# Kernel tuning notes

Measured on AMD Instinct MI355X. Metric: run time of the kernel, lower is better.

Reference implementation:

```python
import jax, jax.numpy as jnp
import numpy as np

C, D, N = 4096, 256, 262144

def setup_inputs() -> dict:
    key = jax.random.key(0)
    k1, k2, k3 = jax.random.split(key, 3)
    centers = jax.random.normal(k1, (C, D), dtype=jnp.float32)
    features = jax.random.normal(k2, (N, D), dtype=jnp.float32)
    labels = jax.random.randint(k3, (N,), 0, C, dtype=jnp.int64)
    return {"centers": centers, "features": features, "labels": labels}

def reference(centers, features, labels):
    # centers: [C, D]; features: [N, D] (unused in forward math); labels: [N]
    c = centers.shape[0]
    sq = jnp.sum(centers * centers, axis=1)                 # [C]
    gram = centers @ centers.T                              # [C, C]
    # pairwise squared euclidean distances; diagonal is exactly 0 analytically
    dist = sq[:, None] + sq[None, :] - 2.0 * gram           # [C, C]
    # centerDist[i] = sum_{j != i} ||c_j - c_i||^2 / (C - 1)
    center_dist = (dist.sum(axis=1) - jnp.diagonal(dist)) / (c - 1)  # [C]
    var = jnp.var(center_dist, ddof=1)                      # torch .var() is unbiased
    return center_dist.sum() / c / var / labels.shape[0]
```

## Files before the change

kernel.cpp:

```cpp
#include <hip/hip_runtime.h>

#define DD 256
#define CC 4096
#define NB 64
#define TPB 1024
#define RPB (CC / NB)
#define D4 (DD / 4)
#define MAGIC 0x05F3A9C1

__global__ __launch_bounds__(TPB) void fused_density(
    const float* __restrict__ centers,
    float* __restrict__ t_part,
    float* __restrict__ S_part,
    double* __restrict__ cd_part,
    double* __restrict__ cd2_part,
    int* __restrict__ flag1,
    int* __restrict__ flag2,
    float* __restrict__ out, long long N) {
  const int tx = threadIdx.x, w = tx >> 6, lane = tx & 63, b = blockIdx.x;

  __shared__ float4 smT[16][64];
  __shared__ float sm2[2][DD];
  __shared__ float smt[DD];
  __shared__ float sSfin;
  __shared__ float sS[16];
  __shared__ double sC[16], sC2[16];
  __shared__ double rc[64], rc2[64];

  const float4* src =
      (const float4*)centers + (size_t)(b * RPB + w * 4) * D4 + lane;
  float4 v0 = src[0 * D4], v1 = src[1 * D4], v2 = src[2 * D4], v3 = src[3 * D4];

  float4 ta;
  ta.x = (v0.x + v1.x) + (v2.x + v3.x);
  ta.y = (v0.y + v1.y) + (v2.y + v3.y);
  ta.z = (v0.z + v1.z) + (v2.z + v3.z);
  ta.w = (v0.w + v1.w) + (v2.w + v3.w);
  smT[w][lane] = ta;
  float ss = (v0.x * v0.x + v0.y * v0.y + v0.z * v0.z + v0.w * v0.w) +
             (v1.x * v1.x + v1.y * v1.y + v1.z * v1.z + v1.w * v1.w) +
             (v2.x * v2.x + v2.y * v2.y + v2.z * v2.z + v2.w * v2.w) +
             (v3.x * v3.x + v3.y * v3.y + v3.z * v3.z + v3.w * v3.w);
  #pragma unroll
  for (int off = 32; off; off >>= 1) ss += __shfl_xor(ss, off, 64);
  if (lane == 0) sS[w] = ss;
  __syncthreads();
  if (tx < 64) {
    float4 s = smT[0][tx];
    #pragma unroll
    for (int k = 1; k < 16; ++k) {
      float4 o = smT[k][tx];
      s.x += o.x; s.y += o.y; s.z += o.z; s.w += o.w;
    }
    ((float4*)t_part)[b * 64 + tx] = s;
  }
  if (tx == 0) {
    float s = 0.f;
    #pragma unroll
    for (int k = 0; k < 16; ++k) s += sS[k];
    S_part[b] = s;
  }
  __syncthreads();
  if (tx == 0)
    __hip_atomic_store(&flag1[b], MAGIC, __ATOMIC_RELEASE,
                       __HIP_MEMORY_SCOPE_AGENT);

  if (tx < NB) {
    while (__hip_atomic_load(&flag1[tx], __ATOMIC_ACQUIRE,
                             __HIP_MEMORY_SCOPE_AGENT) != MAGIC)
      __builtin_amdgcn_s_sleep(1);
  }
  __syncthreads();

  if (tx < 512) {
    const int col = tx & 255, half = tx >> 8;
    const float* tp = t_part + (size_t)half * 32 * DD + col;
    float a0 = 0.f, a1 = 0.f, a2 = 0.f, a3 = 0.f;
    float a4 = 0.f, a5 = 0.f, a6 = 0.f, a7 = 0.f;
    #pragma unroll
    for (int p = 0; p < 32; p += 8) {
      a0 += tp[(p + 0) * DD]; a1 += tp[(p + 1) * DD];
      a2 += tp[(p + 2) * DD]; a3 += tp[(p + 3) * DD];
      a4 += tp[(p + 4) * DD]; a5 += tp[(p + 5) * DD];
      a6 += tp[(p + 6) * DD]; a7 += tp[(p + 7) * DD];
    }
    sm2[half][col] = ((a0 + a1) + (a2 + a3)) + ((a4 + a5) + (a6 + a7));
  } else if (tx >= 512 && tx < 576) {
    float sv = S_part[tx - 512];
    #pragma unroll
    for (int off = 32; off; off >>= 1) sv += __shfl_xor(sv, off, 64);
    if (tx == 512) sSfin = sv;
  }
  __syncthreads();
  if (tx < DD) smt[tx] = sm2[0][tx] + sm2[1][tx];
  __syncthreads();
  const float S = sSfin;
  const float4 t4 = ((const float4*)smt)[lane];

  const float Cf = (float)CC;
  const double inv = 1.0 / (double)(CC - 1);
  double cds = 0.0, cd2 = 0.0;
  #pragma unroll
  for (int r = 0; r < 4; ++r) {
    float4 v = (r == 0) ? v0 : (r == 1) ? v1 : (r == 2) ? v2 : v3;
    float u = (Cf * v.x - 2.f * t4.x) * v.x + (Cf * v.y - 2.f * t4.y) * v.y +
              (Cf * v.z - 2.f * t4.z) * v.z + (Cf * v.w - 2.f * t4.w) * v.w;
    #pragma unroll
    for (int off = 32; off; off >>= 1) u += __shfl_xor(u, off, 64);
    if (lane == 0) {
      double cd = ((double)u + (double)S) * inv;
      cds += cd;
      cd2 += cd * cd;
    }
  }
  if (lane == 0) { sC[w] = cds; sC2[w] = cd2; }
  __syncthreads();
  if (tx == 0) {
    double bc = 0.0, bc2 = 0.0;
    #pragma unroll
    for (int k = 0; k < 16; ++k) { bc += sC[k]; bc2 += sC2[k]; }
    __hip_atomic_store(&cd_part[b], bc, __ATOMIC_RELEASE,
                       __HIP_MEMORY_SCOPE_AGENT);
    __hip_atomic_store(&cd2_part[b], bc2, __ATOMIC_RELEASE,
                       __HIP_MEMORY_SCOPE_AGENT);
    __hip_atomic_store(&flag2[b], MAGIC, __ATOMIC_RELEASE,
                       __HIP_MEMORY_SCOPE_AGENT);
  }

  if (b == 0) {
    if (tx < NB) {
      while (__hip_atomic_load(&flag2[tx], __ATOMIC_ACQUIRE,
                               __HIP_MEMORY_SCOPE_AGENT) != MAGIC)
        __builtin_amdgcn_s_sleep(1);
      rc[tx] = cd_part[tx];
      rc2[tx] = cd2_part[tx];
    }
    __syncthreads();
    #pragma unroll
    for (int st = 32; st; st >>= 1) {
      if (tx < st) { rc[tx] += rc[tx + st]; rc2[tx] += rc2[tx + st]; }
      __syncthreads();
    }
    if (tx == 0) {
      double s = rc[0], s2 = rc2[0];
      double mean = s / (double)CC;
      double var = (s2 - s * s / (double)CC) / (double)(CC - 1);
      out[0] = (float)(mean / var / (double)N);
    }
    if (tx < NB) {
      __hip_atomic_store(&flag1[tx], 0, __ATOMIC_RELEASE,
                         __HIP_MEMORY_SCOPE_AGENT);
      __hip_atomic_store(&flag2[tx], 0, __ATOMIC_RELEASE,
                         __HIP_MEMORY_SCOPE_AGENT);
    }
  }
}

extern "C" void kernel_launch(void* const* d_in, const int* in_sizes, int n_in,
                              void* d_out, int out_size, void* d_ws,
                              size_t ws_size, hipStream_t stream) {
  const float* centers = (const float*)d_in[0];
  long long N = (long long)in_sizes[2];
  (void)n_in; (void)out_size; (void)ws_size;

  char* ws = (char*)d_ws;
  float* t_part = (float*)ws;
  float* S_part = (float*)(ws + 65536);
  double* cd_part = (double*)(ws + 66048);
  double* cd2_part = (double*)(ws + 66560);
  int* flag1 = (int*)(ws + 67072);
  int* flag2 = (int*)(ws + 67328);
  float* outp = (float*)d_out;

  hipLaunchKernelGGL(fused_density, dim3(NB), dim3(TPB), 0, stream, centers,
                     t_part, S_part, cd_part, cd2_part, flag1, flag2, outp, N);
}
```

Before: 16.96 us.

## Use 128 smaller blocks and pack flags with payload in padded cache lines

Doubles the grid to 128 blocks of 512 threads so more CUs load the centers concurrently. Inter-block communication now uses 64-byte-aligned structs that carry each flag next to its payload, which avoids false sharing among flags and lets the payload arrive in the same line as the flag. The cost is a larger grid barrier with twice as many flags to poll, and a longer t_part reduction per thread.

```diff
diff --git a/kernel.cpp b/kernel.cpp
--- a/kernel.cpp
+++ b/kernel.cpp
@@ -2,30 +2,30 @@
 
 #define DD 256
 #define CC 4096
-#define NB 64
-#define TPB 1024
+#define NB 128
+#define TPB 512
 #define RPB (CC / NB)
 #define D4 (DD / 4)
 #define MAGIC 0x05F3A9C1
 
+struct alignas(64) Comm1 { int flag; float S; int pad[14]; };
+struct alignas(64) Comm2 { double cd; double cd2; int flag; int pad[11]; };
+
 __global__ __launch_bounds__(TPB) void fused_density(
     const float* __restrict__ centers,
     float* __restrict__ t_part,
-    float* __restrict__ S_part,
-    double* __restrict__ cd_part,
-    double* __restrict__ cd2_part,
-    int* __restrict__ flag1,
-    int* __restrict__ flag2,
+    Comm1* __restrict__ c1,
+    Comm2* __restrict__ c2,
     float* __restrict__ out, long long N) {
   const int tx = threadIdx.x, w = tx >> 6, lane = tx & 63, b = blockIdx.x;
 
-  __shared__ float4 smT[16][64];
+  __shared__ float4 smT[8][64];
   __shared__ float sm2[2][DD];
   __shared__ float smt[DD];
+  __shared__ float sS[8];
   __shared__ float sSfin;
-  __shared__ float sS[16];
-  __shared__ double sC[16], sC2[16];
-  __shared__ double rc[64], rc2[64];
+  __shared__ double sC[8], sC2[8];
+  __shared__ double rc[NB], rc2[NB];
 
   const float4* src =
       (const float4*)centers + (size_t)(b * RPB + w * 4) * D4 + lane;
@@ -48,7 +48,7 @@
   if (tx < 64) {
     float4 s = smT[0][tx];
     #pragma unroll
-    for (int k = 1; k < 16; ++k) {
+    for (int k = 1; k < 8; ++k) {
       float4 o = smT[k][tx];
       s.x += o.x; s.y += o.y; s.z += o.z; s.w += o.w;
     }
@@ -57,42 +57,44 @@
   if (tx == 0) {
     float s = 0.f;
     #pragma unroll
-    for (int k = 0; k < 16; ++k) s += sS[k];
-    S_part[b] = s;
+    for (int k = 0; k < 8; ++k) s += sS[k];
+    c1[b].S = s;
   }
   __syncthreads();
   if (tx == 0)
-    __hip_atomic_store(&flag1[b], MAGIC, __ATOMIC_RELEASE,
+    __hip_atomic_store(&c1[b].flag, MAGIC, __ATOMIC_RELEASE,
                        __HIP_MEMORY_SCOPE_AGENT);
 
   if (tx < NB) {
-    while (__hip_atomic_load(&flag1[tx], __ATOMIC_ACQUIRE,
+    while (__hip_atomic_load(&c1[tx].flag, __ATOMIC_ACQUIRE,
                              __HIP_MEMORY_SCOPE_AGENT) != MAGIC)
       __builtin_amdgcn_s_sleep(1);
   }
   __syncthreads();
 
-  if (tx < 512) {
+  {
     const int col = tx & 255, half = tx >> 8;
-    const float* tp = t_part + (size_t)half * 32 * DD + col;
+    const float* tp = t_part + (size_t)(half * 64) * DD + col;
     float a0 = 0.f, a1 = 0.f, a2 = 0.f, a3 = 0.f;
     float a4 = 0.f, a5 = 0.f, a6 = 0.f, a7 = 0.f;
     #pragma unroll
-    for (int p = 0; p < 32; p += 8) {
+    for (int p = 0; p < 64; p += 8) {
       a0 += tp[(p + 0) * DD]; a1 += tp[(p + 1) * DD];
       a2 += tp[(p + 2) * DD]; a3 += tp[(p + 3) * DD];
       a4 += tp[(p + 4) * DD]; a5 += tp[(p + 5) * DD];
       a6 += tp[(p + 6) * DD]; a7 += tp[(p + 7) * DD];
     }
     sm2[half][col] = ((a0 + a1) + (a2 + a3)) + ((a4 + a5) + (a6 + a7));
-  } else if (tx >= 512 && tx < 576) {
-    float sv = S_part[tx - 512];
-    #pragma unroll
-    for (int off = 32; off; off >>= 1) sv += __shfl_xor(sv, off, 64);
-    if (tx == 512) sSfin = sv;
   }
   __syncthreads();
   if (tx < DD) smt[tx] = sm2[0][tx] + sm2[1][tx];
+  if (tx >= 256 && tx < 320) {
+    const int l = tx - 256;
+    float sv = c1[l].S + c1[l + 64].S;
+    #pragma unroll
+    for (int off = 32; off; off >>= 1) sv += __shfl_xor(sv, off, 64);
+    if (l == 0) sSfin = sv;
+  }
   __syncthreads();
   const float S = sSfin;
   const float4 t4 = ((const float4*)smt)[lane];
@@ -118,26 +120,24 @@
   if (tx == 0) {
     double bc = 0.0, bc2 = 0.0;
     #pragma unroll
-    for (int k = 0; k < 16; ++k) { bc += sC[k]; bc2 += sC2[k]; }
-    __hip_atomic_store(&cd_part[b], bc, __ATOMIC_RELEASE,
-                       __HIP_MEMORY_SCOPE_AGENT);
-    __hip_atomic_store(&cd2_part[b], bc2, __ATOMIC_RELEASE,
-                       __HIP_MEMORY_SCOPE_AGENT);
-    __hip_atomic_store(&flag2[b], MAGIC, __ATOMIC_RELEASE,
+    for (int k = 0; k < 8; ++k) { bc += sC[k]; bc2 += sC2[k]; }
+    c2[b].cd = bc;
+    c2[b].cd2 = bc2;
+    __hip_atomic_store(&c2[b].flag, MAGIC, __ATOMIC_RELEASE,
                        __HIP_MEMORY_SCOPE_AGENT);
   }
 
   if (b == 0) {
     if (tx < NB) {
-      while (__hip_atomic_load(&flag2[tx], __ATOMIC_ACQUIRE,
+      while (__hip_atomic_load(&c2[tx].flag, __ATOMIC_ACQUIRE,
                                __HIP_MEMORY_SCOPE_AGENT) != MAGIC)
         __builtin_amdgcn_s_sleep(1);
-      rc[tx] = cd_part[tx];
-      rc2[tx] = cd2_part[tx];
+      rc[tx] = c2[tx].cd;
+      rc2[tx] = c2[tx].cd2;
     }
     __syncthreads();
     #pragma unroll
-    for (int st = 32; st; st >>= 1) {
+    for (int st = 64; st; st >>= 1) {
       if (tx < st) { rc[tx] += rc[tx + st]; rc2[tx] += rc2[tx + st]; }
       __syncthreads();
     }
@@ -148,9 +148,9 @@
       out[0] = (float)(mean / var / (double)N);
     }
     if (tx < NB) {
-      __hip_atomic_store(&flag1[tx], 0, __ATOMIC_RELEASE,
+      __hip_atomic_store(&c1[tx].flag, 0, __ATOMIC_RELEASE,
                          __HIP_MEMORY_SCOPE_AGENT);
-      __hip_atomic_store(&flag2[tx], 0, __ATOMIC_RELEASE,
+      __hip_atomic_store(&c2[tx].flag, 0, __ATOMIC_RELEASE,
                          __HIP_MEMORY_SCOPE_AGENT);
     }
   }
@@ -165,13 +165,10 @@
 
   char* ws = (char*)d_ws;
   float* t_part = (float*)ws;
-  float* S_part = (float*)(ws + 65536);
-  double* cd_part = (double*)(ws + 66048);
-  double* cd2_part = (double*)(ws + 66560);
-  int* flag1 = (int*)(ws + 67072);
-  int* flag2 = (int*)(ws + 67328);
+  Comm1* c1 = (Comm1*)(ws + 131072);
+  Comm2* c2 = (Comm2*)(ws + 131072 + 8192);
   float* outp = (float*)d_out;
 
   hipLaunchKernelGGL(fused_density, dim3(NB), dim3(TPB), 0, stream, centers,
-                     t_part, S_part, cd_part, cd2_part, flag1, flag2, outp, N);
+                     t_part, c1, c2, outp, N);
 }
```

Result: slower. 19.32 us (+13.9%).
